# Optimization experiments

Measured on AMD Instinct MI355X. Metric: run time of the kernel, lower is better.

## Reference

```python
import jax, jax.numpy as jnp
import numpy as np

N = 50000      # nodes
E = 800000     # edges (before self loops)
IN = 256       # in_channels
HID = 64       # hidden_channels
HEADS = 2
NEG_SLOPE = 0.2
BN_EPS = 1e-5


def setup_inputs() -> dict:
    key = jax.random.key(0)
    ks = jax.random.split(key, 16)
    def g(i, shape, scale=0.05):
        return jax.random.normal(ks[i], shape, dtype=jnp.float32) * scale
    return {
        "x": jax.random.normal(ks[0], (N, IN), dtype=jnp.float32),
        "edge_index": jax.random.randint(ks[1], (2, E), 0, N, dtype=jnp.int64).astype(jnp.int32),
        # conv1 (GATv2, heads=2, concat)
        "W1l": g(2, (IN, HEADS * HID)), "b1l": jnp.zeros(HEADS * HID, jnp.float32),
        "W1r": g(3, (IN, HEADS * HID)), "b1r": jnp.zeros(HEADS * HID, jnp.float32),
        "att1": g(4, (HEADS, HID)), "bias1": jnp.zeros(HEADS * HID, jnp.float32),
        "bn1_g": jnp.ones(HEADS * HID, jnp.float32), "bn1_b": jnp.zeros(HEADS * HID, jnp.float32),
        "bn1_m": jnp.zeros(HEADS * HID, jnp.float32), "bn1_v": jnp.ones(HEADS * HID, jnp.float32),
        # conv2 (GATv2, heads=1)
        "W2l": g(5, (HEADS * HID, HID)), "b2l": jnp.zeros(HID, jnp.float32),
        "W2r": g(6, (HEADS * HID, HID)), "b2r": jnp.zeros(HID, jnp.float32),
        "att2": g(7, (1, HID)), "bias2": jnp.zeros(HID, jnp.float32),
        "bn2_g": jnp.ones(HID, jnp.float32), "bn2_b": jnp.zeros(HID, jnp.float32),
        "bn2_m": jnp.zeros(HID, jnp.float32), "bn2_v": jnp.ones(HID, jnp.float32),
        # classifier
        "Wc": g(8, (HID, 1)), "bc": jnp.zeros(1, jnp.float32),
    }


def _gatv2(x, src, dst, Wl, bl, Wr, br, att, bias, heads, ch, n):
    # GATv2: e_ij = att . leaky_relu(Wl x_j + Wr x_i); segment softmax over dst; out_i = sum alpha_ij Wl x_j
    xl = (x @ Wl + bl).reshape(n, heads, ch)  # source transform [N,H,C]
    xr = (x @ Wr + br).reshape(n, heads, ch)  # target transform [N,H,C]
    e = jax.nn.leaky_relu(xl[src] + xr[dst], NEG_SLOPE)        # [E,H,C]
    logits = jnp.einsum('ehc,hc->eh', e, att)                  # [E,H]
    m = jax.ops.segment_max(logits, dst, num_segments=n)       # [N,H]
    p = jnp.exp(logits - m[dst])
    s = jax.ops.segment_sum(p, dst, num_segments=n)            # [N,H]
    alpha = p / s[dst]                                         # [E,H]
    out = jax.ops.segment_sum(alpha[:, :, None] * xl[src], dst, num_segments=n)  # [N,H,C]
    return out.reshape(n, heads * ch) + bias


def _bn(x, g, b, m, v):
    return (x - m) * jax.lax.rsqrt(v + BN_EPS) * g + b


def reference(x, edge_index, W1l, b1l, W1r, b1r, att1, bias1,
              bn1_g, bn1_b, bn1_m, bn1_v,
              W2l, b2l, W2r, b2r, att2, bias2,
              bn2_g, bn2_b, bn2_m, bn2_v, Wc, bc):
    n = x.shape[0]
    loop = jnp.arange(n, dtype=edge_index.dtype)  # add_self_loops=True
    src = jnp.concatenate([edge_index[0], loop])
    dst = jnp.concatenate([edge_index[1], loop])
    h = _gatv2(x, src, dst, W1l, b1l, W1r, b1r, att1, bias1, HEADS, HID, n)
    h = jax.nn.elu(_bn(h, bn1_g, bn1_b, bn1_m, bn1_v))
    h = _gatv2(h, src, dst, W2l, b2l, W2r, b2r, att2, bias2, 1, HID, n)
    h = jax.nn.elu(_bn(h, bn2_g, bn2_b, bn2_m, bn2_v))
    return jax.nn.sigmoid(h @ Wc + bc)
```

## Files before the change

### kernel.cpp

```cpp
#include <hip/hip_runtime.h>
#include <hip/hip_bf16.h>
#include <cstddef>

#define NN 50000
#define EE 800000
#define TE 850000
#define INC 256
#define C1 128
#define C2 64
#define NCHUNK 49

#define NB_COUNT 3321
#define NB_GEMM1 782
#define NB_K1    (NB_GEMM1 + NB_COUNT)
#define NB_Z     196
#define NB_PREP0 (NB_Z + 256 + 128)

#define LOG2E 1.44269504088896340736f

typedef unsigned short ushort_t;
typedef short bf16x8 __attribute__((ext_vector_type(8)));
typedef float f32x4 __attribute__((ext_vector_type(4)));

__device__ inline ushort_t bf16r(float f) {
    unsigned u = __float_as_uint(f);
    unsigned r = (u + 0x7fffu + ((u >> 16) & 1u)) >> 16;
    return (ushort_t)r;
}
__device__ inline unsigned packbf2(float a, float b) {
    return (unsigned)bf16r(a) | ((unsigned)bf16r(b) << 16);
}
#define LOF(u) (__uint_as_float((u) << 16))
#define HIF(u) (__uint_as_float((u) & 0xffff0000u))
#define ELU(t) ((t) > 0.f ? (t) : (__expf(t) - 1.f))

__device__ inline void unpack8(const uint4& u, float f[8]) {
    f[0] = LOF(u.x); f[1] = HIF(u.x);
    f[2] = LOF(u.y); f[3] = HIF(u.y);
    f[4] = LOF(u.z); f[5] = HIF(u.z);
    f[6] = LOF(u.w); f[7] = HIF(u.w);
}


__global__ void k_scan1(const int* __restrict__ deg, int* __restrict__ incl,
                        int* __restrict__ totals) {
    __shared__ int lds[1024];
    int t = threadIdx.x;
    int i = blockIdx.x * 1024 + t;
    int v = (i < NN) ? deg[i] : 0;
    lds[t] = v;
    __syncthreads();
    for (int off = 1; off < 1024; off <<= 1) {
        int add = (t >= off) ? lds[t - off] : 0;
        __syncthreads();
        lds[t] += add;
        __syncthreads();
    }
    if (i < NN) incl[i] = lds[t];
    if (t == 1023) totals[blockIdx.x] = lds[t];
}

__global__ void k_scan3(const int* __restrict__ incl, const int* __restrict__ deg,
                        const int* __restrict__ totals, int* __restrict__ rowstart) {
    int i = blockIdx.x * blockDim.x + threadIdx.x;
    if (i == 0) rowstart[NN] = TE;
    if (i >= NN) return;
    int chunk = blockIdx.x >> 2;
    int coff = 0;
    for (int c = 0; c < chunk; c++) coff += totals[c];
    rowstart[i] = incl[i] - deg[i] + coff;
}


__global__ __launch_bounds__(256) void k_prep0(
    int* __restrict__ deg,
    const float* __restrict__ W1l, const float* __restrict__ W1r,
    const float* __restrict__ b1l, const float* __restrict__ b1r,
    ushort_t* __restrict__ Wt1, float* __restrict__ biasf1,
    const float* __restrict__ W2l, const float* __restrict__ W2r,
    const float* __restrict__ b2l, const float* __restrict__ b2r,
    ushort_t* __restrict__ Wt2, float* __restrict__ biasf2) {
    int b = blockIdx.x, tid = threadIdx.x;
    if (b < NB_Z) {
        int i = b * 256 + tid;
        if (i < NN) deg[i] = 0;
    } else if (b < NB_Z + 256) {
        int n = b - NB_Z;
        int k = tid;
        const float* W = (n < 128) ? W1l : W1r;
        int c = (n < 128) ? n : n - 128;
        Wt1[(size_t)n * 256 + k] = bf16r(W[(size_t)k * 128 + c]);
        if (n == 0) biasf1[k] = (k < 128) ? b1l[k] : b1r[k - 128];
    } else {
        int n = b - NB_Z - 256;
        int k = tid;
        if (k < 128) {
            const float* W = (n < 64) ? W2l : W2r;
            int c = (n < 64) ? n : n - 64;
            Wt2[(size_t)n * 128 + k] = bf16r(W[(size_t)k * 64 + c]);
            if (n == 0) biasf2[k] = (k < 64) ? b2l[k] : b2r[k - 64];
        }
    }
}


template <int K, int NCOL, bool AF32>
__device__ inline void gemm_body(const void* __restrict__ Aptr,
                                 const ushort_t* __restrict__ Bt,
                                 const float* __restrict__ bias,
                                 ushort_t* __restrict__ C, int M,
                                 int bm, int bn, ushort_t* As, ushort_t* Bs) {
    int tid = threadIdx.x;
    int w = tid >> 6, l = tid & 63;
    int wm = (w & 1) * 64, wn = (w >> 1) * 64;
    int lm = l & 15, half = l >> 4;

    f32x4 zero = {0.f, 0.f, 0.f, 0.f};
    f32x4 acc[4][4];
#pragma unroll
    for (int a = 0; a < 4; a++)
#pragma unroll
        for (int b = 0; b < 4; b++) acc[a][b] = zero;

    for (int k0 = 0; k0 < K; k0 += 32) {
#pragma unroll
        for (int q = 0; q < 2; q++) {
            int seg = q * 256 + tid;
            int mrow = seg >> 2;
            int ko = (seg & 3) * 8;
            if constexpr (AF32) {
                const float* A = (const float*)Aptr;
                int r = bm + mrow;
                if (r > M - 1) r = M - 1;
                const float* ap = &A[(size_t)r * K + k0 + ko];
                float4 lo = *(const float4*)ap;
                float4 hi = *(const float4*)(ap + 4);
                uint4 pk;
                pk.x = packbf2(lo.x, lo.y); pk.y = packbf2(lo.z, lo.w);
                pk.z = packbf2(hi.x, hi.y); pk.w = packbf2(hi.z, hi.w);
                *(uint4*)&As[mrow * 40 + ko] = pk;
            } else {
                const ushort_t* A = (const ushort_t*)Aptr;
                *(float4*)&As[mrow * 40 + ko] =
                    *(const float4*)&A[(size_t)(bm + mrow) * K + k0 + ko];
            }
            *(float4*)&Bs[mrow * 40 + ko] = *(const float4*)&Bt[(size_t)(bn + mrow) * K + k0 + ko];
        }
        __syncthreads();
        bf16x8 af[4], bfr[4];
#pragma unroll
        for (int mi = 0; mi < 4; mi++)
            af[mi] = *(const bf16x8*)&As[(wm + mi * 16 + lm) * 40 + half * 8];
#pragma unroll
        for (int ni = 0; ni < 4; ni++)
            bfr[ni] = *(const bf16x8*)&Bs[(wn + ni * 16 + lm) * 40 + half * 8];
#pragma unroll
        for (int mi = 0; mi < 4; mi++)
#pragma unroll
            for (int ni = 0; ni < 4; ni++)
                acc[mi][ni] = __builtin_amdgcn_mfma_f32_16x16x32_bf16(
                    af[mi], bfr[ni], acc[mi][ni], 0, 0, 0);
        __syncthreads();
    }
#pragma unroll
    for (int ni = 0; ni < 4; ni++) {
        int col = bn + wn + ni * 16 + lm;
        float bv = bias[col];
#pragma unroll
        for (int mi = 0; mi < 4; mi++) {
            int rbase = bm + wm + mi * 16 + half * 4;
#pragma unroll
            for (int r = 0; r < 4; r++) {
                int row = rbase + r;
                if (row < M) C[(size_t)row * NCOL + col] = bf16r(acc[mi][ni][r] + bv);
            }
        }
    }
}


__global__ __launch_bounds__(256) void k_stage1(
    const int* __restrict__ ei, int* __restrict__ deg, int* __restrict__ rank,
    const float* __restrict__ x, const ushort_t* __restrict__ Wt1,
    const float* __restrict__ biasf1, ushort_t* __restrict__ xlr1) {
    int b = blockIdx.x;
    if (b < NB_GEMM1) {
        __shared__ __align__(16) ushort_t As[128 * 40];
        __shared__ __align__(16) ushort_t Bs[128 * 40];
        int bm = (b >> 1) * 128;
        int bn = (b & 1) * 128;
        gemm_body<256, 256, true>(x, Wt1, biasf1, xlr1, NN, bm, bn, As, Bs);
    } else {
        int e = (b - NB_GEMM1) * 256 + threadIdx.x;
        if (e < TE) {
            int dst = (e < EE) ? ei[EE + e] : (e - EE);
            rank[e] = atomicAdd(&deg[dst], 1);
        }
    }
}


__global__ __launch_bounds__(256) void k_scatter(
    const int* __restrict__ ei, const int* __restrict__ rank,
    const int* __restrict__ rowstart, int* __restrict__ ssrc) {
    int e = blockIdx.x * 256 + threadIdx.x;
    if (e < TE) {
        int s, d;
        if (e < EE) { s = ei[e]; d = ei[EE + e]; }
        else        { s = e - EE; d = s; }
        ssrc[rowstart[d] + rank[e]] = s;
    }
}

__global__ __launch_bounds__(256) void k_gemm2(
    const ushort_t* __restrict__ A, const ushort_t* __restrict__ Bt,
    const float* __restrict__ bias, ushort_t* __restrict__ C) {
    __shared__ __align__(16) ushort_t As[128 * 40];
    __shared__ __align__(16) ushort_t Bs[128 * 40];
    int bm = blockIdx.x * 128;
    gemm_body<128, 128, false>(A, Bt, bias, C, NN, bm, 0, As, Bs);
}


__global__ __launch_bounds__(256) void k_fused1(
    const ushort_t* __restrict__ xlr, const int* __restrict__ rowstart,
    const int* __restrict__ ssrc, const float* __restrict__ att,
    const float* __restrict__ bias,
    const float* __restrict__ g, const float* __restrict__ b,
    const float* __restrict__ m, const float* __restrict__ v,
    ushort_t* __restrict__ out) {
    int lane = threadIdx.x & 63;
    int i = blockIdx.x * 4 + (threadIdx.x >> 6);
    if (i >= NN) return;
    int slot = lane >> 4;
    int c8 = lane & 15;
    const char* xb = (const char*)xlr;
    unsigned coff = (unsigned)c8 << 4;
    float xr[8];
    { uint4 u = *(const uint4*)(xb + (((unsigned)i << 9) + 256u + coff)); unpack8(u, xr); }
    float a6[8], a4[8];
    {
        const float* ap = att + 8 * c8;
#pragma unroll
        for (int c = 0; c < 8; c++) {
            float a = ap[c];
            a6[c] = a * (0.6f * LOG2E);
            a4[c] = a * (0.4f * LOG2E);
        }
    }
    int row = rowstart[i], end = rowstart[i + 1];
    float acc[8] = {0.f, 0.f, 0.f, 0.f, 0.f, 0.f, 0.f, 0.f};
    float s = 0.f;
    int j = row;
    for (; j + 16 <= end; j += 16) {
        int src[4];
        uint4 u[4];
#pragma unroll
        for (int k = 0; k < 4; k++) src[k] = ssrc[j + 4 * k + slot];
#pragma unroll
        for (int k = 0; k < 4; k++)
            u[k] = *(const uint4*)(xb + (((unsigned)src[k] << 9) + coff));
#pragma unroll
        for (int k = 0; k < 4; k++) {
            float f[8];
            unpack8(u[k], f);
            float t0 = f[0] + xr[0];
            float dd = fmaf(a6[0], t0, a4[0] * fabsf(t0));
#pragma unroll
            for (int c = 1; c < 8; c++) {
                float t = f[c] + xr[c];
                dd = fmaf(a6[c], t, fmaf(a4[c], fabsf(t), dd));
            }
            dd += __shfl_xor(dd, 1, 64);
            dd += __shfl_xor(dd, 2, 64);
            dd += __shfl_xor(dd, 4, 64);
            float p = exp2f(dd);
            s += p;
#pragma unroll
            for (int c = 0; c < 8; c++) acc[c] = fmaf(p, f[c], acc[c]);
        }
    }
    for (; j < end; j += 4) {
        int je = j + slot;
        bool valid = je < end;
        int src = valid ? ssrc[je] : i;
        uint4 uu = *(const uint4*)(xb + (((unsigned)src << 9) + coff));
        float f[8];
        unpack8(uu, f);
        float t0 = f[0] + xr[0];
        float dd = fmaf(a6[0], t0, a4[0] * fabsf(t0));
#pragma unroll
        for (int c = 1; c < 8; c++) {
            float t = f[c] + xr[c];
            dd = fmaf(a6[c], t, fmaf(a4[c], fabsf(t), dd));
        }
        dd += __shfl_xor(dd, 1, 64);
        dd += __shfl_xor(dd, 2, 64);
        dd += __shfl_xor(dd, 4, 64);
        float p = valid ? exp2f(dd) : 0.f;
        s += p;
#pragma unroll
        for (int c = 0; c < 8; c++) acc[c] = fmaf(p, f[c], acc[c]);
    }
#pragma unroll
    for (int o = 16; o <= 32; o <<= 1) {
#pragma unroll
        for (int c = 0; c < 8; c++) acc[c] += __shfl_xor(acc[c], o, 64);
        s += __shfl_xor(s, o, 64);
    }
    if (slot == 0) {
        float inv = 1.f / s;
        const float* bp = bias + 8 * c8;
        const float* mp = m + 8 * c8;
        const float* vp = v + 8 * c8;
        const float* gp = g + 8 * c8;
        const float* b2p = b + 8 * c8;
        unsigned ov[4];
#pragma unroll
        for (int c = 0; c < 8; c += 2) {
            float o0 = acc[c] * inv + bp[c];
            float o1 = acc[c + 1] * inv + bp[c + 1];
            o0 = (o0 - mp[c]) * rsqrtf(vp[c] + 1e-5f) * gp[c] + b2p[c];
            o1 = (o1 - mp[c + 1]) * rsqrtf(vp[c + 1] + 1e-5f) * gp[c + 1] + b2p[c + 1];
            o0 = ELU(o0); o1 = ELU(o1);
            ov[c >> 1] = (unsigned)bf16r(o0) | ((unsigned)bf16r(o1) << 16);
        }
        uint4 w4;
        w4.x = ov[0]; w4.y = ov[1]; w4.z = ov[2]; w4.w = ov[3];
        *(uint4*)((char*)out + (((unsigned)i << 8) + coff)) = w4;
    }
}


__global__ __launch_bounds__(256) void k_fused2(
    const ushort_t* __restrict__ xlr, const int* __restrict__ rowstart,
    const int* __restrict__ ssrc, const float* __restrict__ att,
    const float* __restrict__ bias,
    const float* __restrict__ g, const float* __restrict__ b,
    const float* __restrict__ m, const float* __restrict__ v,
    const float* __restrict__ Wc, const float* __restrict__ bc,
    float* __restrict__ out) {
    int lane = threadIdx.x & 63;
    int i = blockIdx.x * 4 + (threadIdx.x >> 6);
    if (i >= NN) return;
    int slot = lane >> 3;
    int c8 = lane & 7;
    const char* xb = (const char*)xlr;
    unsigned coff = (unsigned)c8 << 4;
    float xr[8];
    { uint4 u = *(const uint4*)(xb + (((unsigned)i << 8) + 128u + coff)); unpack8(u, xr); }
    float a6[8], a4[8];
    {
        const float* ap = att + 8 * c8;
#pragma unroll
        for (int c = 0; c < 8; c++) {
            float a = ap[c];
            a6[c] = a * (0.6f * LOG2E);
            a4[c] = a * (0.4f * LOG2E);
        }
    }
    int row = rowstart[i], end = rowstart[i + 1];
    float acc[8] = {0.f, 0.f, 0.f, 0.f, 0.f, 0.f, 0.f, 0.f};
    float s = 0.f;
    int j = row;
    for (; j + 16 <= end; j += 16) {
        int src[2];
        uint4 u[2];
#pragma unroll
        for (int k = 0; k < 2; k++) src[k] = ssrc[j + 8 * k + slot];
#pragma unroll
        for (int k = 0; k < 2; k++)
            u[k] = *(const uint4*)(xb + (((unsigned)src[k] << 8) + coff));
#pragma unroll
        for (int k = 0; k < 2; k++) {
            float f[8];
            unpack8(u[k], f);
            float t0 = f[0] + xr[0];
            float dd = fmaf(a6[0], t0, a4[0] * fabsf(t0));
#pragma unroll
            for (int c = 1; c < 8; c++) {
                float t = f[c] + xr[c];
                dd = fmaf(a6[c], t, fmaf(a4[c], fabsf(t), dd));
            }
            dd += __shfl_xor(dd, 1, 64);
            dd += __shfl_xor(dd, 2, 64);
            dd += __shfl_xor(dd, 4, 64);
            float p = exp2f(dd);
            s += p;
#pragma unroll
            for (int c = 0; c < 8; c++) acc[c] = fmaf(p, f[c], acc[c]);
        }
    }
    for (; j < end; j += 8) {
        int je = j + slot;
        bool valid = je < end;
        int src = valid ? ssrc[je] : i;
        uint4 uu = *(const uint4*)(xb + (((unsigned)src << 8) + coff));
        float f[8];
        unpack8(uu, f);
        float t0 = f[0] + xr[0];
        float dd = fmaf(a6[0], t0, a4[0] * fabsf(t0));
#pragma unroll
        for (int c = 1; c < 8; c++) {
            float t = f[c] + xr[c];
            dd = fmaf(a6[c], t, fmaf(a4[c], fabsf(t), dd));
        }
        dd += __shfl_xor(dd, 1, 64);
        dd += __shfl_xor(dd, 2, 64);
        dd += __shfl_xor(dd, 4, 64);
        float p = valid ? exp2f(dd) : 0.f;
        s += p;
#pragma unroll
        for (int c = 0; c < 8; c++) acc[c] = fmaf(p, f[c], acc[c]);
    }
#pragma unroll
    for (int o = 8; o <= 32; o <<= 1) {
#pragma unroll
        for (int c = 0; c < 8; c++) acc[c] += __shfl_xor(acc[c], o, 64);
        s += __shfl_xor(s, o, 64);
    }
    float inv = 1.f / s;
    const float* bp = bias + 8 * c8;
    const float* mp = m + 8 * c8;
    const float* vp = v + 8 * c8;
    const float* gp = g + 8 * c8;
    const float* b2p = b + 8 * c8;
    const float* wp = Wc + 8 * c8;
    float z = 0.f;
#pragma unroll
    for (int c = 0; c < 8; c++) {
        float o0 = acc[c] * inv + bp[c];
        o0 = (o0 - mp[c]) * rsqrtf(vp[c] + 1e-5f) * gp[c] + b2p[c];
        o0 = ELU(o0);
        z = fmaf(o0, wp[c], z);
    }
    z += __shfl_xor(z, 1, 64);
    z += __shfl_xor(z, 2, 64);
    z += __shfl_xor(z, 4, 64);
    if (lane == 0) out[i] = 1.f / (1.f + __expf(-(z + bc[0])));
}


extern "C" void kernel_launch(void* const* d_in, const int* in_sizes, int n_in,
                              void* d_out, int out_size, void* d_ws, size_t ws_size,
                              hipStream_t stream) {
    const float* x    = (const float*)d_in[0];
    const int*   ei   = (const int*)d_in[1];
    const float* W1l  = (const float*)d_in[2];
    const float* b1l  = (const float*)d_in[3];
    const float* W1r  = (const float*)d_in[4];
    const float* b1r  = (const float*)d_in[5];
    const float* att1 = (const float*)d_in[6];
    const float* bias1= (const float*)d_in[7];
    const float* bn1g = (const float*)d_in[8];
    const float* bn1b = (const float*)d_in[9];
    const float* bn1m = (const float*)d_in[10];
    const float* bn1v = (const float*)d_in[11];
    const float* W2l  = (const float*)d_in[12];
    const float* b2l  = (const float*)d_in[13];
    const float* W2r  = (const float*)d_in[14];
    const float* b2r  = (const float*)d_in[15];
    const float* att2 = (const float*)d_in[16];
    const float* bias2= (const float*)d_in[17];
    const float* bn2g = (const float*)d_in[18];
    const float* bn2b = (const float*)d_in[19];
    const float* bn2m = (const float*)d_in[20];
    const float* bn2v = (const float*)d_in[21];
    const float* Wc   = (const float*)d_in[22];
    const float* bc   = (const float*)d_in[23];
    float* out = (float*)d_out;

    char* ws = (char*)d_ws;
    size_t off = 0;
    auto alloc = [&](size_t bytes) {
        size_t o = off;
        off += (bytes + 255) & ~(size_t)255;
        return o;
    };
    ushort_t* xlr1  = (ushort_t*)(ws + alloc((size_t)NN * 256 * 2));
    ushort_t* h1b   = (ushort_t*)(ws + alloc((size_t)(NN + 128) * 128 * 2));
    ushort_t* Wt1   = (ushort_t*)(ws + alloc((size_t)256 * 256 * 2));
    float*    biasf1= (float*)(ws + alloc(256 * 4));
    ushort_t* Wt2   = (ushort_t*)(ws + alloc((size_t)128 * 128 * 2));
    float*    biasf2= (float*)(ws + alloc(128 * 4));
    int* deg      = (int*)(ws + alloc((size_t)NN * 4));
    int* incl     = (int*)(ws + alloc((size_t)NN * 4));
    int* rowstart = (int*)(ws + alloc((size_t)(NN + 1) * 4));
    int* totals   = (int*)(ws + alloc(64 * 4));
    int* rank     = (int*)(ws + alloc((size_t)TE * 4));
    int* ssrc     = (int*)(ws + alloc((size_t)TE * 4));
    ushort_t* xlr2 = xlr1;

    k_prep0<<<NB_PREP0, 256, 0, stream>>>(deg, W1l, W1r, b1l, b1r, Wt1, biasf1,
                                          W2l, W2r, b2l, b2r, Wt2, biasf2);

    k_stage1<<<NB_K1, 256, 0, stream>>>(ei, deg, rank, x, Wt1, biasf1, xlr1);

    k_scan1<<<NCHUNK, 1024, 0, stream>>>(deg, incl, totals);
    k_scan3<<<(NN + 255) / 256, 256, 0, stream>>>(incl, deg, totals, rowstart);

    k_scatter<<<NB_COUNT, 256, 0, stream>>>(ei, rank, rowstart, ssrc);

    k_fused1<<<(NN + 3) / 4, 256, 0, stream>>>(xlr1, rowstart, ssrc, att1, bias1,
                                               bn1g, bn1b, bn1m, bn1v, h1b);

    k_gemm2<<<(NN + 127) / 128, 256, 0, stream>>>(h1b, Wt2, biasf2, xlr2);
    k_fused2<<<(NN + 3) / 4, 256, 0, stream>>>(xlr2, rowstart, ssrc, att2, bias2,
                                               bn2g, bn2b, bn2m, bn2v, Wc, bc, out);
}
```

Measured before the change: 307.6 us.

## Register-prefetch GEMM tiles, vectorize degree count and scatter, reorder stage1 blocks

The GEMM body now loads the next K-tile from global memory into registers while MFMAs run on the current LDS tile, which hides global latency in a software pipeline. The degree-count and CSR-scatter kernels each handle four edges per thread through int4 loads, so they launch a quarter as many threads and issue wider memory accesses. Stage1 puts the count blocks ahead of the GEMM blocks so the atomic counting is dispatched first. The prefetch adds register pressure, and packing four atomics per thread gives less parallelism per atomic.

After: 350.3 us. 1.14x slower.

```diff
diff --git a/kernel.cpp b/kernel.cpp
--- a/kernel.cpp
+++ b/kernel.cpp
@@ -10,9 +10,11 @@
 #define C2 64
 #define NCHUNK 49
 
-#define NB_COUNT 3321
+#define QTE 212500
+#define QEE 200000
+#define NB_CNT 831
 #define NB_GEMM1 782
-#define NB_K1    (NB_GEMM1 + NB_COUNT)
+#define NB_K1    (NB_CNT + NB_GEMM1)
 #define NB_Z     196
 #define NB_PREP0 (NB_Z + 256 + 128)
 
@@ -114,6 +116,53 @@
     int w = tid >> 6, l = tid & 63;
     int wm = (w & 1) * 64, wn = (w >> 1) * 64;
     int lm = l & 15, half = l >> 4;
+    constexpr int NT = K / 32;
+
+    int mrow[2], koff[2];
+#pragma unroll
+    for (int q = 0; q < 2; q++) {
+        int seg = q * 256 + tid;
+        mrow[q] = seg >> 2;
+        koff[q] = (seg & 3) * 8;
+    }
+
+    float4 areg[2][2];
+    float4 breg[2];
+
+    auto load_tile = [&](int kt) {
+        int k0 = kt * 32;
+#pragma unroll
+        for (int q = 0; q < 2; q++) {
+            if constexpr (AF32) {
+                const float* A = (const float*)Aptr;
+                int r = bm + mrow[q];
+                if (r > M - 1) r = M - 1;
+                const float* ap = &A[(size_t)r * K + k0 + koff[q]];
+                areg[q][0] = *(const float4*)ap;
+                areg[q][1] = *(const float4*)(ap + 4);
+            } else {
+                const ushort_t* A = (const ushort_t*)Aptr;
+                areg[q][0] = *(const float4*)&A[(size_t)(bm + mrow[q]) * K + k0 + koff[q]];
+            }
+            breg[q] = *(const float4*)&Bt[(size_t)(bn + mrow[q]) * K + k0 + koff[q]];
+        }
+    };
+    auto write_tile = [&]() {
+#pragma unroll
+        for (int q = 0; q < 2; q++) {
+            if constexpr (AF32) {
+                uint4 pk;
+                pk.x = packbf2(areg[q][0].x, areg[q][0].y);
+                pk.y = packbf2(areg[q][0].z, areg[q][0].w);
+                pk.z = packbf2(areg[q][1].x, areg[q][1].y);
+                pk.w = packbf2(areg[q][1].z, areg[q][1].w);
+                *(uint4*)&As[mrow[q] * 40 + koff[q]] = pk;
+            } else {
+                *(float4*)&As[mrow[q] * 40 + koff[q]] = areg[q][0];
+            }
+            *(float4*)&Bs[mrow[q] * 40 + koff[q]] = breg[q];
+        }
+    };
 
     f32x4 zero = {0.f, 0.f, 0.f, 0.f};
     f32x4 acc[4][4];
@@ -122,31 +171,11 @@
 #pragma unroll
         for (int b = 0; b < 4; b++) acc[a][b] = zero;
 
-    for (int k0 = 0; k0 < K; k0 += 32) {
-#pragma unroll
-        for (int q = 0; q < 2; q++) {
-            int seg = q * 256 + tid;
-            int mrow = seg >> 2;
-            int ko = (seg & 3) * 8;
-            if constexpr (AF32) {
-                const float* A = (const float*)Aptr;
-                int r = bm + mrow;
-                if (r > M - 1) r = M - 1;
-                const float* ap = &A[(size_t)r * K + k0 + ko];
-                float4 lo = *(const float4*)ap;
-                float4 hi = *(const float4*)(ap + 4);
-                uint4 pk;
-                pk.x = packbf2(lo.x, lo.y); pk.y = packbf2(lo.z, lo.w);
-                pk.z = packbf2(hi.x, hi.y); pk.w = packbf2(hi.z, hi.w);
-                *(uint4*)&As[mrow * 40 + ko] = pk;
-            } else {
-                const ushort_t* A = (const ushort_t*)Aptr;
-                *(float4*)&As[mrow * 40 + ko] =
-                    *(const float4*)&A[(size_t)(bm + mrow) * K + k0 + ko];
-            }
-            *(float4*)&Bs[mrow * 40 + ko] = *(const float4*)&Bt[(size_t)(bn + mrow) * K + k0 + ko];
-        }
+    load_tile(0);
+    for (int kt = 0; kt < NT; kt++) {
+        write_tile();
         __syncthreads();
+        if (kt + 1 < NT) load_tile(kt + 1);
         bf16x8 af[4], bfr[4];
 #pragma unroll
         for (int mi = 0; mi < 4; mi++)
@@ -184,18 +213,32 @@
     const float* __restrict__ x, const ushort_t* __restrict__ Wt1,
     const float* __restrict__ biasf1, ushort_t* __restrict__ xlr1) {
     int b = blockIdx.x;
-    if (b < NB_GEMM1) {
+    if (b < NB_CNT) {
+        int t = b * 256 + threadIdx.x;
+        if (t < QEE) {
+            int4 d4 = ((const int4*)(ei + EE))[t];
+            int4 r4;
+            r4.x = atomicAdd(&deg[d4.x], 1);
+            r4.y = atomicAdd(&deg[d4.y], 1);
+            r4.z = atomicAdd(&deg[d4.z], 1);
+            r4.w = atomicAdd(&deg[d4.w], 1);
+            ((int4*)rank)[t] = r4;
+        } else if (t < QTE) {
+            int n0 = 4 * t - EE;
+            int4 r4;
+            r4.x = atomicAdd(&deg[n0], 1);
+            r4.y = atomicAdd(&deg[n0 + 1], 1);
+            r4.z = atomicAdd(&deg[n0 + 2], 1);
+            r4.w = atomicAdd(&deg[n0 + 3], 1);
+            ((int4*)rank)[t] = r4;
+        }
+    } else {
         __shared__ __align__(16) ushort_t As[128 * 40];
         __shared__ __align__(16) ushort_t Bs[128 * 40];
-        int bm = (b >> 1) * 128;
-        int bn = (b & 1) * 128;
+        int g = b - NB_CNT;
+        int bm = (g >> 1) * 128;
+        int bn = (g & 1) * 128;
         gemm_body<256, 256, true>(x, Wt1, biasf1, xlr1, NN, bm, bn, As, Bs);
-    } else {
-        int e = (b - NB_GEMM1) * 256 + threadIdx.x;
-        if (e < TE) {
-            int dst = (e < EE) ? ei[EE + e] : (e - EE);
-            rank[e] = atomicAdd(&deg[dst], 1);
-        }
     }
 }
 
@@ -203,12 +246,22 @@
 __global__ __launch_bounds__(256) void k_scatter(
     const int* __restrict__ ei, const int* __restrict__ rank,
     const int* __restrict__ rowstart, int* __restrict__ ssrc) {
-    int e = blockIdx.x * 256 + threadIdx.x;
-    if (e < TE) {
-        int s, d;
-        if (e < EE) { s = ei[e]; d = ei[EE + e]; }
-        else        { s = e - EE; d = s; }
-        ssrc[rowstart[d] + rank[e]] = s;
+    int t = blockIdx.x * 256 + threadIdx.x;
+    if (t < QEE) {
+        int4 s4 = ((const int4*)ei)[t];
+        int4 d4 = ((const int4*)(ei + EE))[t];
+        int4 r4 = ((const int4*)rank)[t];
+        ssrc[rowstart[d4.x] + r4.x] = s4.x;
+        ssrc[rowstart[d4.y] + r4.y] = s4.y;
+        ssrc[rowstart[d4.z] + r4.z] = s4.z;
+        ssrc[rowstart[d4.w] + r4.w] = s4.w;
+    } else if (t < QTE) {
+        int n0 = 4 * t - EE;
+        int4 r4 = ((const int4*)rank)[t];
+        ssrc[rowstart[n0] + r4.x] = n0;
+        ssrc[rowstart[n0 + 1] + r4.y] = n0 + 1;
+        ssrc[rowstart[n0 + 2] + r4.z] = n0 + 2;
+        ssrc[rowstart[n0 + 3] + r4.w] = n0 + 3;
     }
 }
 
@@ -499,7 +552,7 @@
     k_scan1<<<NCHUNK, 1024, 0, stream>>>(deg, incl, totals);
     k_scan3<<<(NN + 255) / 256, 256, 0, stream>>>(incl, deg, totals, rowstart);
 
-    k_scatter<<<NB_COUNT, 256, 0, stream>>>(ei, rank, rowstart, ssrc);
+    k_scatter<<<NB_CNT, 256, 0, stream>>>(ei, rank, rowstart, ssrc);
 
     k_fused1<<<(NN + 3) / 4, 256, 0, stream>>>(xlr1, rowstart, ssrc, att1, bias1,
                                                bn1g, bn1b, bn1m, bn1v, h1b);
```

## Pre-cast x to bf16 and fuse GEMM1 with CSR scatter kernel

Applied to the files above, without the earlier changes.

Moves the fp32-to-bf16 conversion of x out of the GEMM into a separate cast pass that shares a launch with degree counting and weight transposes. GEMM1 is moved to run alongside the edge scatter in one launch, and the degree zeroing becomes a memset. This regroups work across stages so independent jobs overlap and the GEMM loads bf16 directly. The cost is an extra write and read of a 25 MB bf16 copy of x, plus an additional memset call.

Measured after the change: 321.6 us. 4.5% more time.

```diff
diff --git a/kernel.cpp b/kernel.cpp
--- a/kernel.cpp
+++ b/kernel.cpp
@@ -11,10 +11,12 @@
 #define NCHUNK 49
 
 #define NB_COUNT 3321
+#define NB_CAST  12500
+#define NB_P1    256
+#define NB_P2    128
+#define NB_K1    (NB_COUNT + NB_CAST + NB_P1 + NB_P2)
 #define NB_GEMM1 782
-#define NB_K1    (NB_GEMM1 + NB_COUNT)
-#define NB_Z     196
-#define NB_PREP0 (NB_Z + 256 + 128)
+#define NB_K2    (NB_GEMM1 + NB_COUNT)
 
 #define LOG2E 1.44269504088896340736f
 
@@ -26,9 +28,6 @@
     unsigned u = __float_as_uint(f);
     unsigned r = (u + 0x7fffu + ((u >> 16) & 1u)) >> 16;
     return (ushort_t)r;
-}
-__device__ inline unsigned packbf2(float a, float b) {
-    return (unsigned)bf16r(a) | ((unsigned)bf16r(b) << 16);
 }
 #define LOF(u) (__uint_as_float((u) << 16))
 #define HIF(u) (__uint_as_float((u) & 0xffff0000u))
@@ -72,27 +71,38 @@
 }
 
 
-__global__ __launch_bounds__(256) void k_prep0(
-    int* __restrict__ deg,
+__global__ __launch_bounds__(256) void k_stage1(
+    const int* __restrict__ ei, int* __restrict__ deg, int* __restrict__ rank,
+    const float* __restrict__ x, ushort_t* __restrict__ xb,
     const float* __restrict__ W1l, const float* __restrict__ W1r,
     const float* __restrict__ b1l, const float* __restrict__ b1r,
     ushort_t* __restrict__ Wt1, float* __restrict__ biasf1,
     const float* __restrict__ W2l, const float* __restrict__ W2r,
     const float* __restrict__ b2l, const float* __restrict__ b2r,
     ushort_t* __restrict__ Wt2, float* __restrict__ biasf2) {
-    int b = blockIdx.x, tid = threadIdx.x;
-    if (b < NB_Z) {
-        int i = b * 256 + tid;
-        if (i < NN) deg[i] = 0;
-    } else if (b < NB_Z + 256) {
-        int n = b - NB_Z;
+    int b = blockIdx.x;
+    int tid = threadIdx.x;
+    if (b < NB_COUNT) {
+        int e = b * 256 + tid;
+        if (e < TE) {
+            int dst = (e < EE) ? ei[EE + e] : (e - EE);
+            rank[e] = atomicAdd(&deg[dst], 1);
+        }
+    } else if (b < NB_COUNT + NB_CAST) {
+        int i = (b - NB_COUNT) * 256 + tid;
+        float4 a = ((const float4*)x)[i];
+        ushort4 o;
+        o.x = bf16r(a.x); o.y = bf16r(a.y); o.z = bf16r(a.z); o.w = bf16r(a.w);
+        ((ushort4*)xb)[i] = o;
+    } else if (b < NB_COUNT + NB_CAST + NB_P1) {
+        int n = b - NB_COUNT - NB_CAST;
         int k = tid;
         const float* W = (n < 128) ? W1l : W1r;
         int c = (n < 128) ? n : n - 128;
         Wt1[(size_t)n * 256 + k] = bf16r(W[(size_t)k * 128 + c]);
         if (n == 0) biasf1[k] = (k < 128) ? b1l[k] : b1r[k - 128];
     } else {
-        int n = b - NB_Z - 256;
+        int n = b - NB_COUNT - NB_CAST - NB_P1;
         int k = tid;
         if (k < 128) {
             const float* W = (n < 64) ? W2l : W2r;
@@ -104,8 +114,8 @@
 }
 
 
-template <int K, int NCOL, bool AF32>
-__device__ inline void gemm_body(const void* __restrict__ Aptr,
+template <int K, int NCOL>
+__device__ inline void gemm_body(const ushort_t* __restrict__ A,
                                  const ushort_t* __restrict__ Bt,
                                  const float* __restrict__ bias,
                                  ushort_t* __restrict__ C, int M,
@@ -126,25 +136,10 @@
 #pragma unroll
         for (int q = 0; q < 2; q++) {
             int seg = q * 256 + tid;
-            int mrow = seg >> 2;
+            int m = seg >> 2;
             int ko = (seg & 3) * 8;
-            if constexpr (AF32) {
-                const float* A = (const float*)Aptr;
-                int r = bm + mrow;
-                if (r > M - 1) r = M - 1;
-                const float* ap = &A[(size_t)r * K + k0 + ko];
-                float4 lo = *(const float4*)ap;
-                float4 hi = *(const float4*)(ap + 4);
-                uint4 pk;
-                pk.x = packbf2(lo.x, lo.y); pk.y = packbf2(lo.z, lo.w);
-                pk.z = packbf2(hi.x, hi.y); pk.w = packbf2(hi.z, hi.w);
-                *(uint4*)&As[mrow * 40 + ko] = pk;
-            } else {
-                const ushort_t* A = (const ushort_t*)Aptr;
-                *(float4*)&As[mrow * 40 + ko] =
-                    *(const float4*)&A[(size_t)(bm + mrow) * K + k0 + ko];
-            }
-            *(float4*)&Bs[mrow * 40 + ko] = *(const float4*)&Bt[(size_t)(bn + mrow) * K + k0 + ko];
+            *(float4*)&As[m * 40 + ko] = *(const float4*)&A[(size_t)(bm + m) * K + k0 + ko];
+            *(float4*)&Bs[m * 40 + ko] = *(const float4*)&Bt[(size_t)(bn + m) * K + k0 + ko];
         }
         __syncthreads();
         bf16x8 af[4], bfr[4];
@@ -179,36 +174,26 @@
 }
 
 
-__global__ __launch_bounds__(256) void k_stage1(
-    const int* __restrict__ ei, int* __restrict__ deg, int* __restrict__ rank,
-    const float* __restrict__ x, const ushort_t* __restrict__ Wt1,
-    const float* __restrict__ biasf1, ushort_t* __restrict__ xlr1) {
+__global__ __launch_bounds__(256) void k_gemm1_scatter(
+    const ushort_t* __restrict__ A, const ushort_t* __restrict__ Bt,
+    const float* __restrict__ bias, ushort_t* __restrict__ C,
+    const int* __restrict__ ei, const int* __restrict__ rank,
+    const int* __restrict__ rowstart, int* __restrict__ ssrc) {
+    __shared__ __align__(16) ushort_t As[128 * 40];
+    __shared__ __align__(16) ushort_t Bs[128 * 40];
     int b = blockIdx.x;
     if (b < NB_GEMM1) {
-        __shared__ __align__(16) ushort_t As[128 * 40];
-        __shared__ __align__(16) ushort_t Bs[128 * 40];
         int bm = (b >> 1) * 128;
         int bn = (b & 1) * 128;
-        gemm_body<256, 256, true>(x, Wt1, biasf1, xlr1, NN, bm, bn, As, Bs);
+        gemm_body<256, 256>(A, Bt, bias, C, NN, bm, bn, As, Bs);
     } else {
         int e = (b - NB_GEMM1) * 256 + threadIdx.x;
         if (e < TE) {
-            int dst = (e < EE) ? ei[EE + e] : (e - EE);
-            rank[e] = atomicAdd(&deg[dst], 1);
-        }
-    }
-}
-
-
-__global__ __launch_bounds__(256) void k_scatter(
-    const int* __restrict__ ei, const int* __restrict__ rank,
-    const int* __restrict__ rowstart, int* __restrict__ ssrc) {
-    int e = blockIdx.x * 256 + threadIdx.x;
-    if (e < TE) {
-        int s, d;
-        if (e < EE) { s = ei[e]; d = ei[EE + e]; }
-        else        { s = e - EE; d = s; }
-        ssrc[rowstart[d] + rank[e]] = s;
+            int s, d;
+            if (e < EE) { s = ei[e]; d = ei[EE + e]; }
+            else        { s = e - EE; d = s; }
+            ssrc[rowstart[d] + rank[e]] = s;
+        }
     }
 }
 
@@ -218,7 +203,7 @@
     __shared__ __align__(16) ushort_t As[128 * 40];
     __shared__ __align__(16) ushort_t Bs[128 * 40];
     int bm = blockIdx.x * 128;
-    gemm_body<128, 128, false>(A, Bt, bias, C, NN, bm, 0, As, Bs);
+    gemm_body<128, 128>(A, Bt, bias, C, NN, bm, 0, As, Bs);
 }
 
 
@@ -477,6 +462,7 @@
         off += (bytes + 255) & ~(size_t)255;
         return o;
     };
+    ushort_t* xb    = (ushort_t*)(ws + alloc((size_t)(NN + 128) * 256 * 2));
     ushort_t* xlr1  = (ushort_t*)(ws + alloc((size_t)NN * 256 * 2));
     ushort_t* h1b   = (ushort_t*)(ws + alloc((size_t)(NN + 128) * 128 * 2));
     ushort_t* Wt1   = (ushort_t*)(ws + alloc((size_t)256 * 256 * 2));
@@ -491,15 +477,17 @@
     int* ssrc     = (int*)(ws + alloc((size_t)TE * 4));
     ushort_t* xlr2 = xlr1;
 
-    k_prep0<<<NB_PREP0, 256, 0, stream>>>(deg, W1l, W1r, b1l, b1r, Wt1, biasf1,
-                                          W2l, W2r, b2l, b2r, Wt2, biasf2);
-
-    k_stage1<<<NB_K1, 256, 0, stream>>>(ei, deg, rank, x, Wt1, biasf1, xlr1);
+    hipMemsetAsync(deg, 0, (size_t)NN * 4, stream);
+
+    k_stage1<<<NB_K1, 256, 0, stream>>>(ei, deg, rank, x, xb,
+                                        W1l, W1r, b1l, b1r, Wt1, biasf1,
+                                        W2l, W2r, b2l, b2r, Wt2, biasf2);
 
     k_scan1<<<NCHUNK, 1024, 0, stream>>>(deg, incl, totals);
     k_scan3<<<(NN + 255) / 256, 256, 0, stream>>>(incl, deg, totals, rowstart);
 
-    k_scatter<<<NB_COUNT, 256, 0, stream>>>(ei, rank, rowstart, ssrc);
+    k_gemm1_scatter<<<NB_K2, 256, 0, stream>>>(xb, Wt1, biasf1, xlr1,
+                                               ei, rank, rowstart, ssrc);
 
     k_fused1<<<(NN + 3) / 4, 256, 0, stream>>>(xlr1, rowstart, ssrc, att1, bias1,
                                                bn1g, bn1b, bn1m, bn1v, h1b);
```
